# Performance work log

Hardware: AMD Instinct MI355X
Metric: run time of the kernel (lower is better)

Reference implementation:

```python
import jax, jax.numpy as jnp
import numpy as np

N_NODES = 100000


def _gcn_conv(x, W, b, src, dst, norm):
    # x: [N, Fin] -> [N, Fout]; PyG GCNConv: linear, normalized scatter-add, bias
    x = x @ W
    msgs = x[src] * norm[:, None]  # gather + edge scale
    out = jax.ops.segment_sum(msgs, dst, num_segments=N_NODES)
    return out + b


def setup_inputs() -> dict:
    key = jax.random.key(0)
    ks = jax.random.split(key, 8)
    N, E, F, H, C = N_NODES, 600000, 128, 128, 40
    s = lambda fan: 1.0 / np.sqrt(fan)
    return {
        "features": jax.random.normal(ks[0], (N, F), dtype=jnp.float32),
        "edge_index": jax.random.randint(ks[1], (2, E), 0, N, dtype=jnp.int64),
        "W1": jax.random.normal(ks[2], (F, H), dtype=jnp.float32) * s(F),
        "b1": jnp.zeros((H,), dtype=jnp.float32),
        "W2": jax.random.normal(ks[3], (H, H), dtype=jnp.float32) * s(H),
        "b2": jnp.zeros((H,), dtype=jnp.float32),
        "W3": jax.random.normal(ks[4], (H, C), dtype=jnp.float32) * s(H),
        "b3": jnp.zeros((C,), dtype=jnp.float32),
    }


def reference(features, edge_index, W1, b1, W2, b2, W3, b3):
    N = N_NODES
    # add self-loops (PyG GCNConv default)
    loops = jnp.arange(N, dtype=edge_index.dtype)
    src = jnp.concatenate([edge_index[0], loops])
    dst = jnp.concatenate([edge_index[1], loops])
    # symmetric normalization: deg^-1/2[src] * deg^-1/2[dst]
    deg = jax.ops.segment_sum(jnp.ones_like(dst, dtype=features.dtype), dst,
                              num_segments=N)
    dis = jnp.where(deg > 0, jax.lax.rsqrt(jnp.maximum(deg, 1.0)), 0.0)
    norm = dis[src] * dis[dst]

    x = jax.nn.relu(_gcn_conv(features, W1, b1, src, dst, norm))
    x = jax.nn.relu(_gcn_conv(x, W2, b2, src, dst, norm))
    x = jax.nn.relu(_gcn_conv(x, W3, b3, src, dst, norm))
    return jax.nn.log_softmax(x, axis=-1)
```

## Files before the change

### kernel.cpp

```cpp
#include <hip/hip_runtime.h>
#include <hip/hip_bf16.h>

#define NN 100000
#define NE 600000
#define NBLK 391
#define NPAD 100096

typedef unsigned int uint;
typedef unsigned short ushort;
typedef __attribute__((ext_vector_type(8))) short bf16x8;
typedef __attribute__((ext_vector_type(4))) float f32x4;

__device__ __forceinline__ ushort f2b(float f) {
    union { float f; uint u; } v; v.f = f;
    return (ushort)((v.u + 0x7fffu + ((v.u >> 16) & 1u)) >> 16);
}
__device__ __forceinline__ float b2f(uint h) {
    union { uint u; float f; } v; v.u = h << 16; return v.f;
}

__global__ __launch_bounds__(256) void k_cnt_init(int* __restrict__ cnt) {
    int i = blockIdx.x * 256 + threadIdx.x;
    if (i < NN) cnt[i] = 0;
}
__global__ __launch_bounds__(256) void k_cnt(const int* __restrict__ dst,
                                             int* __restrict__ cnt) {
    int e = blockIdx.x * 256 + threadIdx.x;
    if (e < NE) atomicAdd(&cnt[dst[e]], 1);
}
__global__ __launch_bounds__(256) void k_blockred(const int* __restrict__ cnt,
                                                  int* __restrict__ blocksum) {
    int t = threadIdx.x;
    int i = blockIdx.x * 256 + t;
    int c = (i < NN) ? cnt[i] : 0;
    #pragma unroll
    for (int o = 32; o; o >>= 1) c += __shfl_xor(c, o, 64);
    __shared__ int ws[4];
    if ((t & 63) == 0) ws[t >> 6] = c;
    __syncthreads();
    if (t == 0) blocksum[blockIdx.x] = ws[0] + ws[1] + ws[2] + ws[3];
}
__global__ __launch_bounds__(256) void k_scanblk(const int* __restrict__ blocksum,
                                                 int* __restrict__ blockbase) {
    __shared__ int s[NBLK];
    int t = threadIdx.x;
    for (int i = t; i < NBLK; i += 256) s[i] = blocksum[i];
    __syncthreads();
    if (t == 0) {
        int run = 0;
        for (int i = 0; i < NBLK; ++i) { int v = s[i]; s[i] = run; run += v; }
    }
    __syncthreads();
    for (int i = t; i < NBLK; i += 256) blockbase[i] = s[i];
}
__global__ __launch_bounds__(256) void k_offsets(const int* __restrict__ cnt,
                                                 const int* __restrict__ blockbase,
                                                 int* __restrict__ offsets,
                                                 int* __restrict__ cursor,
                                                 float* __restrict__ dis) {
    int t = threadIdx.x, lane = t & 63, wv = t >> 6;
    int i = blockIdx.x * 256 + t;
    int c = (i < NN) ? cnt[i] : 0;
    int x = c;
    #pragma unroll
    for (int o = 1; o < 64; o <<= 1) {
        int v = __shfl_up(x, o, 64);
        if (lane >= o) x += v;
    }
    __shared__ int wsum[4], wbase[4];
    if (lane == 63) wsum[wv] = x;
    __syncthreads();
    if (t == 0) {
        int run = 0;
        #pragma unroll
        for (int k = 0; k < 4; ++k) { wbase[k] = run; run += wsum[k]; }
    }
    __syncthreads();
    int excl = blockbase[blockIdx.x] + wbase[wv] + x - c;
    if (i < NN) {
        offsets[i] = excl;
        cursor[i] = excl;
        dis[i] = rsqrtf((float)(c + 1));
        if (i == NN - 1) offsets[NN] = excl + c;
    }
}
__global__ __launch_bounds__(256) void k_fill(const int* __restrict__ src,
                                              const int* __restrict__ dst,
                                              const float* __restrict__ dis,
                                              int* __restrict__ cursor,
                                              int2* __restrict__ edges) {
    int e = blockIdx.x * 256 + threadIdx.x;
    if (e < NE) {
        int s = src[e], d = dst[e];
        int pos = atomicAdd(&cursor[d], 1);
        float nr = dis[s] * dis[d];
        edges[pos] = make_int2(s, __float_as_int(nr));
    }
}

__global__ __launch_bounds__(256) void k_castW(const float* __restrict__ W1,
                                               const float* __restrict__ W2,
                                               const float* __restrict__ W3,
                                               ushort* __restrict__ WTall) {
    int o = blockIdx.x * 256 + threadIdx.x;
    if (o >= 38912) return;
    float v;
    if (o < 32768) {
        const float* W = (o < 16384) ? W1 : W2;
        int off = o & 16383;
        int n = off >> 7, k = off & 127;
        v = W[k * 128 + n];
    } else {
        int off = o - 32768;
        int n = off >> 7, k = off & 127;
        v = (n < 40) ? W3[k * 40 + n] : 0.f;
    }
    WTall[o] = f2b(v);
}

template <bool F32IN>
__global__ __launch_bounds__(256) void k_gemm128b(const void* __restrict__ Xin,
                                                  const ushort* __restrict__ WT,
                                                  ushort* __restrict__ Yb) {
    __shared__ ushort AL[64 * 136];
    __shared__ ushort BL[128 * 136];
    const int t = threadIdx.x;
    const int rbase = blockIdx.x * 64;
    #pragma unroll
    for (int i = 0; i < 8; ++i) {
        int ch = t + 256 * i;
        int n = ch >> 4, c = ch & 15;
        *(int4*)(BL + n * 136 + c * 8) = *(const int4*)(WT + n * 128 + c * 8);
    }
    #pragma unroll
    for (int i = 0; i < 4; ++i) {
        int ch = t + 256 * i;
        int m = ch >> 4, c = ch & 15;
        int row = min(rbase + m, NN - 1);
        if (F32IN) {
            const float* Xf = (const float*)Xin;
            float4 f0 = *(const float4*)(Xf + (size_t)row * 128 + c * 8);
            float4 f1 = *(const float4*)(Xf + (size_t)row * 128 + c * 8 + 4);
            ushort* p = AL + m * 136 + c * 8;
            p[0] = f2b(f0.x); p[1] = f2b(f0.y); p[2] = f2b(f0.z); p[3] = f2b(f0.w);
            p[4] = f2b(f1.x); p[5] = f2b(f1.y); p[6] = f2b(f1.z); p[7] = f2b(f1.w);
        } else {
            const ushort* Xb = (const ushort*)Xin;
            *(int4*)(AL + m * 136 + c * 8) =
                *(const int4*)(Xb + (size_t)row * 128 + c * 8);
        }
    }
    __syncthreads();
    const int wv = t >> 6, l = t & 63;
    const int m16 = l & 15, q = l >> 4;
    f32x4 acc[8];
    #pragma unroll
    for (int j = 0; j < 8; ++j) acc[j] = (f32x4){0.f, 0.f, 0.f, 0.f};
    #pragma unroll
    for (int kt = 0; kt < 4; ++kt) {
        bf16x8 a = *(const bf16x8*)(AL + (wv * 16 + m16) * 136 + kt * 32 + q * 8);
        #pragma unroll
        for (int j = 0; j < 8; ++j) {
            bf16x8 b = *(const bf16x8*)(BL + (j * 16 + m16) * 136 + kt * 32 + q * 8);
            acc[j] = __builtin_amdgcn_mfma_f32_16x16x32_bf16(a, b, acc[j], 0, 0, 0);
        }
    }
    #pragma unroll
    for (int r = 0; r < 4; ++r) {
        int row = rbase + wv * 16 + q * 4 + r;
        if (row < NN) {
            #pragma unroll
            for (int j = 0; j < 8; ++j)
                Yb[(size_t)row * 128 + j * 16 + m16] = f2b(acc[j][r]);
        }
    }
}

__global__ __launch_bounds__(256) void k_gemm40b(const ushort* __restrict__ Xb,
                                                 const ushort* __restrict__ W3T,
                                                 ushort* __restrict__ Yb) {
    __shared__ ushort AL[128 * 136];
    __shared__ ushort BL[48 * 136];
    const int t = threadIdx.x;
    const int rbase = blockIdx.x * 128;
    #pragma unroll
    for (int i = 0; i < 3; ++i) {
        int ch = t + 256 * i;
        int n = ch >> 4, c = ch & 15;
        *(int4*)(BL + n * 136 + c * 8) = *(const int4*)(W3T + n * 128 + c * 8);
    }
    #pragma unroll
    for (int i = 0; i < 8; ++i) {
        int ch = t + 256 * i;
        int m = ch >> 4, c = ch & 15;
        *(int4*)(AL + m * 136 + c * 8) =
            *(const int4*)(Xb + (size_t)(rbase + m) * 128 + c * 8);
    }
    __syncthreads();
    const int wv = t >> 6, l = t & 63;
    const int m16 = l & 15, q = l >> 4;
    f32x4 acc[2][3];
    #pragma unroll
    for (int i = 0; i < 2; ++i)
        #pragma unroll
        for (int j = 0; j < 3; ++j) acc[i][j] = (f32x4){0.f, 0.f, 0.f, 0.f};
    #pragma unroll
    for (int kt = 0; kt < 4; ++kt) {
        bf16x8 a[2], b[3];
        #pragma unroll
        for (int i = 0; i < 2; ++i)
            a[i] = *(const bf16x8*)(AL + ((wv * 2 + i) * 16 + m16) * 136 + kt * 32 + q * 8);
        #pragma unroll
        for (int j = 0; j < 3; ++j)
            b[j] = *(const bf16x8*)(BL + (j * 16 + m16) * 136 + kt * 32 + q * 8);
        #pragma unroll
        for (int i = 0; i < 2; ++i)
            #pragma unroll
            for (int j = 0; j < 3; ++j)
                acc[i][j] = __builtin_amdgcn_mfma_f32_16x16x32_bf16(a[i], b[j], acc[i][j], 0, 0, 0);
    }
    #pragma unroll
    for (int i = 0; i < 2; ++i) {
        #pragma unroll
        for (int r = 0; r < 4; ++r) {
            int row = rbase + (wv * 2 + i) * 16 + q * 4 + r;
            if (row < NN) {
                #pragma unroll
                for (int j = 0; j < 3; ++j)
                    Yb[(size_t)row * 64 + j * 16 + m16] = f2b(acc[i][j][r]);
            }
        }
    }
}

__global__ __launch_bounds__(256) void k_agg128b(const int* __restrict__ offsets,
                                                 const int2* __restrict__ edges,
                                                 const float* __restrict__ dis,
                                                 const ushort* __restrict__ xw,
                                                 const float* __restrict__ bias,
                                                 ushort* __restrict__ out) {
    const int t = threadIdx.x;
    const int wv = t >> 6, lane = t & 63;
    const int hl = lane & 31;
    const int hsel = lane & 32;
    const int n = (blockIdx.x * 4 + wv) * 2 + (lane >> 5);
    const bool nvalid = n < NN;
    const int nc = nvalid ? n : NN - 1;
    const int beg = offsets[nc], end = offsets[nc + 1];
    const int deg = end - beg;
    int2 em = (hl < deg) ? edges[beg + hl] : make_int2(0, 0);
    int s_l = em.x;
    float w_l = __int_as_float(em.y);
    float d = dis[nc];
    uint2 v0 = ((const uint2*)(xw + (size_t)nc * 128))[hl];
    float a0 = b2f(v0.x & 0xffffu) * (d * d);
    float a1 = b2f(v0.x >> 16) * (d * d);
    float a2 = b2f(v0.y & 0xffffu) * (d * d);
    float a3 = b2f(v0.y >> 16) * (d * d);
    int degc = min(deg, 32);
    int dmax = max(degc, __shfl_xor(degc, 32, 64));
    int jceil = (dmax + 7) & ~7;
    for (int j = 0; j < jceil; j += 8) {
        int s[8]; float w[8]; uint2 u[8];
        #pragma unroll
        for (int k = 0; k < 8; ++k) {
            s[k] = __shfl(s_l, hsel + j + k, 64);
            w[k] = __shfl(w_l, hsel + j + k, 64);
        }
        #pragma unroll
        for (int k = 0; k < 8; ++k)
            u[k] = ((const uint2*)(xw + (size_t)s[k] * 128))[hl];
        #pragma unroll
        for (int k = 0; k < 8; ++k) {
            a0 = fmaf(b2f(u[k].x & 0xffffu), w[k], a0);
            a1 = fmaf(b2f(u[k].x >> 16), w[k], a1);
            a2 = fmaf(b2f(u[k].y & 0xffffu), w[k], a2);
            a3 = fmaf(b2f(u[k].y >> 16), w[k], a3);
        }
    }
    for (int jj = beg + 32; jj < end; ++jj) {
        int2 e2 = edges[jj];
        float w = __int_as_float(e2.y);
        uint2 u = ((const uint2*)(xw + (size_t)e2.x * 128))[hl];
        a0 = fmaf(b2f(u.x & 0xffffu), w, a0);
        a1 = fmaf(b2f(u.x >> 16), w, a1);
        a2 = fmaf(b2f(u.y & 0xffffu), w, a2);
        a3 = fmaf(b2f(u.y >> 16), w, a3);
    }
    float4 bv = ((const float4*)bias)[hl];
    a0 = fmaxf(a0 + bv.x, 0.f);
    a1 = fmaxf(a1 + bv.y, 0.f);
    a2 = fmaxf(a2 + bv.z, 0.f);
    a3 = fmaxf(a3 + bv.w, 0.f);
    if (nvalid) {
        uint2 o;
        o.x = (uint)f2b(a0) | ((uint)f2b(a1) << 16);
        o.y = (uint)f2b(a2) | ((uint)f2b(a3) << 16);
        ((uint2*)(out + (size_t)n * 128))[hl] = o;
    }
}

__global__ __launch_bounds__(256) void k_agg40_lsm(const int* __restrict__ offsets,
                                                   const int2* __restrict__ edges,
                                                   const float* __restrict__ dis,
                                                   const ushort* __restrict__ xw,
                                                   const float* __restrict__ bias,
                                                   float* __restrict__ out) {
    const int t = threadIdx.x;
    const int wv = t >> 6, lane = t & 63;
    const int hl = lane & 31;
    const int hsel = lane & 32;
    const int n = (blockIdx.x * 4 + wv) * 2 + (lane >> 5);
    const bool nvalid = n < NN;
    const int nc = nvalid ? n : NN - 1;
    const bool act = hl < 20;
    const int beg = offsets[nc], end = offsets[nc + 1];
    const int deg = end - beg;
    int2 em = (hl < deg) ? edges[beg + hl] : make_int2(0, 0);
    int s_l = em.x;
    float w_l = __int_as_float(em.y);
    float d = dis[nc];
    uint v0 = ((const uint*)(xw + (size_t)nc * 64))[hl];
    float x0 = b2f(v0 & 0xffffu) * (d * d);
    float x1 = b2f(v0 >> 16) * (d * d);
    int degc = min(deg, 32);
    int dmax = max(degc, __shfl_xor(degc, 32, 64));
    int jceil = (dmax + 7) & ~7;
    for (int j = 0; j < jceil; j += 8) {
        int s[8]; float w[8]; uint u[8];
        #pragma unroll
        for (int k = 0; k < 8; ++k) {
            s[k] = __shfl(s_l, hsel + j + k, 64);
            w[k] = __shfl(w_l, hsel + j + k, 64);
        }
        #pragma unroll
        for (int k = 0; k < 8; ++k)
            u[k] = ((const uint*)(xw + (size_t)s[k] * 64))[hl];
        #pragma unroll
        for (int k = 0; k < 8; ++k) {
            x0 = fmaf(b2f(u[k] & 0xffffu), w[k], x0);
            x1 = fmaf(b2f(u[k] >> 16), w[k], x1);
        }
    }
    for (int jj = beg + 32; jj < end; ++jj) {
        int2 e2 = edges[jj];
        float w = __int_as_float(e2.y);
        uint u = ((const uint*)(xw + (size_t)e2.x * 64))[hl];
        x0 = fmaf(b2f(u & 0xffffu), w, x0);
        x1 = fmaf(b2f(u >> 16), w, x1);
    }
    if (act) {
        float2 bv = ((const float2*)bias)[hl];
        x0 = fmaxf(x0 + bv.x, 0.f);
        x1 = fmaxf(x1 + bv.y, 0.f);
    }
    float m = act ? fmaxf(x0, x1) : -1e30f;
    #pragma unroll
    for (int o = 16; o; o >>= 1) m = fmaxf(m, __shfl_xor(m, o, 64));
    float e = act ? (expf(x0 - m) + expf(x1 - m)) : 0.f;
    #pragma unroll
    for (int o = 16; o; o >>= 1) e += __shfl_xor(e, o, 64);
    if (act && nvalid) {
        float lg = m + logf(e);
        float2 o2 = make_float2(x0 - lg, x1 - lg);
        *(float2*)(out + (size_t)n * 40 + 2 * hl) = o2;
    }
}

extern "C" void kernel_launch(void* const* d_in, const int* in_sizes, int n_in,
                              void* d_out, int out_size, void* d_ws, size_t ws_size,
                              hipStream_t stream) {
    const float* feat = (const float*)d_in[0];
    const int* ei = (const int*)d_in[1];
    const float* W1 = (const float*)d_in[2];
    const float* b1 = (const float*)d_in[3];
    const float* W2 = (const float*)d_in[4];
    const float* b2 = (const float*)d_in[5];
    const float* W3 = (const float*)d_in[6];
    const float* b3 = (const float*)d_in[7];
    const int* src = ei;
    const int* dst = ei + NE;
    float* out = (float*)d_out;

    char* w = (char*)d_ws;
    int* cnt = (int*)w;        w += 100352 * 4;
    float* dis = (float*)w;    w += 100352 * 4;
    int* offsets = (int*)w;    w += 100608 * 4;
    int* cursor = (int*)w;     w += 100352 * 4;
    int* blocksum = (int*)w;   w += 512 * 4;
    int* blockbase = (int*)w;  w += 512 * 4;
    int2* edges = (int2*)w;    w += 600064 * 8;
    ushort* WTall = (ushort*)w; w += 39168 * 2;
    ushort* W1T = WTall;
    ushort* W2T = WTall + 16384;
    ushort* W3T = WTall + 32768;
    ushort* bufYb = (ushort*)w; w += (size_t)NPAD * 128 * 2;
    ushort* bufXb = (ushort*)w; w += (size_t)NPAD * 128 * 2;
    ushort* Y40b = (ushort*)w;  w += (size_t)NPAD * 64 * 2;

    const int B = 256;
    #define CDIV(a, b) (((a) + (b) - 1) / (b))

    k_cnt_init<<<NBLK, B, 0, stream>>>(cnt);
    k_cnt<<<CDIV(NE, B), B, 0, stream>>>(dst, cnt);
    k_blockred<<<NBLK, B, 0, stream>>>(cnt, blocksum);
    k_scanblk<<<1, B, 0, stream>>>(blocksum, blockbase);
    k_offsets<<<NBLK, B, 0, stream>>>(cnt, blockbase, offsets, cursor, dis);
    k_fill<<<CDIV(NE, B), B, 0, stream>>>(src, dst, dis, cursor, edges);
    k_castW<<<CDIV(38912, B), B, 0, stream>>>(W1, W2, W3, WTall);

    k_gemm128b<true><<<CDIV(NN, 64), B, 0, stream>>>(feat, W1T, bufYb);
    k_agg128b<<<CDIV(NN, 8), B, 0, stream>>>(offsets, edges, dis, bufYb, b1, bufXb);
    k_gemm128b<false><<<CDIV(NN, 64), B, 0, stream>>>(bufXb, W2T, bufYb);
    k_agg128b<<<CDIV(NN, 8), B, 0, stream>>>(offsets, edges, dis, bufYb, b2, bufXb);
    k_gemm40b<<<CDIV(NN, 128), B, 0, stream>>>(bufXb, W3T, Y40b);
    k_agg40_lsm<<<CDIV(NN, 8), B, 0, stream>>>(offsets, edges, dis, Y40b, b3, out);
    #undef CDIV
}
```

Baseline: 279.1 us.

## Use 16 lanes per node in 128-wide aggregation, fuse castW into scan kernel

The 128-feature aggregation kernel now assigns 16 lanes per node instead of 32, with each lane loading 16-byte (uint4) bf16 chunks and accumulating 8 features, so one wave handles four nodes. The edge window preloaded into lanes shrinks from 32 to 16, and higher-degree tails fall back to a serial loop. The weight cast kernel is merged into the single-block scan kernel as extra blocks to save a launch, and the fp32-to-bf16 staging in the first GEMM writes one 16-byte shared store instead of eight scalar stores. The wider per-lane gathers should cut instruction count per byte, at the cost of more work per lane and more nodes spilling into the serial tail loop.

```diff
diff --git a/kernel.cpp b/kernel.cpp
--- a/kernel.cpp
+++ b/kernel.cpp
@@ -14,6 +14,9 @@
 __device__ __forceinline__ ushort f2b(float f) {
     union { float f; uint u; } v; v.f = f;
     return (ushort)((v.u + 0x7fffu + ((v.u >> 16) & 1u)) >> 16);
+}
+__device__ __forceinline__ uint f2b2(float lo, float hi) {
+    return (uint)f2b(lo) | ((uint)f2b(hi) << 16);
 }
 __device__ __forceinline__ float b2f(uint h) {
     union { uint u; float f; } v; v.u = h << 16; return v.f;
@@ -40,18 +43,39 @@
     __syncthreads();
     if (t == 0) blocksum[blockIdx.x] = ws[0] + ws[1] + ws[2] + ws[3];
 }
-__global__ __launch_bounds__(256) void k_scanblk(const int* __restrict__ blocksum,
-                                                 int* __restrict__ blockbase) {
-    __shared__ int s[NBLK];
+__global__ __launch_bounds__(256) void k_scanblk_castW(const int* __restrict__ blocksum,
+                                                       int* __restrict__ blockbase,
+                                                       const float* __restrict__ W1,
+                                                       const float* __restrict__ W2,
+                                                       const float* __restrict__ W3,
+                                                       ushort* __restrict__ WTall) {
     int t = threadIdx.x;
-    for (int i = t; i < NBLK; i += 256) s[i] = blocksum[i];
-    __syncthreads();
-    if (t == 0) {
-        int run = 0;
-        for (int i = 0; i < NBLK; ++i) { int v = s[i]; s[i] = run; run += v; }
-    }
-    __syncthreads();
-    for (int i = t; i < NBLK; i += 256) blockbase[i] = s[i];
+    if (blockIdx.x == 0) {
+        __shared__ int s[NBLK];
+        for (int i = t; i < NBLK; i += 256) s[i] = blocksum[i];
+        __syncthreads();
+        if (t == 0) {
+            int run = 0;
+            for (int i = 0; i < NBLK; ++i) { int v = s[i]; s[i] = run; run += v; }
+        }
+        __syncthreads();
+        for (int i = t; i < NBLK; i += 256) blockbase[i] = s[i];
+    } else {
+        int o = (blockIdx.x - 1) * 256 + t;
+        if (o >= 38912) return;
+        float v;
+        if (o < 32768) {
+            const float* W = (o < 16384) ? W1 : W2;
+            int off = o & 16383;
+            int n = off >> 7, k = off & 127;
+            v = W[k * 128 + n];
+        } else {
+            int off = o - 32768;
+            int n = off >> 7, k = off & 127;
+            v = (n < 40) ? W3[k * 40 + n] : 0.f;
+        }
+        WTall[o] = f2b(v);
+    }
 }
 __global__ __launch_bounds__(256) void k_offsets(const int* __restrict__ cnt,
                                                  const int* __restrict__ blockbase,
@@ -98,26 +122,6 @@
     }
 }
 
-__global__ __launch_bounds__(256) void k_castW(const float* __restrict__ W1,
-                                               const float* __restrict__ W2,
-                                               const float* __restrict__ W3,
-                                               ushort* __restrict__ WTall) {
-    int o = blockIdx.x * 256 + threadIdx.x;
-    if (o >= 38912) return;
-    float v;
-    if (o < 32768) {
-        const float* W = (o < 16384) ? W1 : W2;
-        int off = o & 16383;
-        int n = off >> 7, k = off & 127;
-        v = W[k * 128 + n];
-    } else {
-        int off = o - 32768;
-        int n = off >> 7, k = off & 127;
-        v = (n < 40) ? W3[k * 40 + n] : 0.f;
-    }
-    WTall[o] = f2b(v);
-}
-
 template <bool F32IN>
 __global__ __launch_bounds__(256) void k_gemm128b(const void* __restrict__ Xin,
                                                   const ushort* __restrict__ WT,
@@ -141,9 +145,12 @@
             const float* Xf = (const float*)Xin;
             float4 f0 = *(const float4*)(Xf + (size_t)row * 128 + c * 8);
             float4 f1 = *(const float4*)(Xf + (size_t)row * 128 + c * 8 + 4);
-            ushort* p = AL + m * 136 + c * 8;
-            p[0] = f2b(f0.x); p[1] = f2b(f0.y); p[2] = f2b(f0.z); p[3] = f2b(f0.w);
-            p[4] = f2b(f1.x); p[5] = f2b(f1.y); p[6] = f2b(f1.z); p[7] = f2b(f1.w);
+            uint4 o;
+            o.x = f2b2(f0.x, f0.y);
+            o.y = f2b2(f0.z, f0.w);
+            o.z = f2b2(f1.x, f1.y);
+            o.w = f2b2(f1.z, f1.w);
+            *(uint4*)(AL + m * 136 + c * 8) = o;
         } else {
             const ushort* Xb = (const ushort*)Xin;
             *(int4*)(AL + m * 136 + c * 8) =
@@ -241,9 +248,9 @@
                                                  ushort* __restrict__ out) {
     const int t = threadIdx.x;
     const int wv = t >> 6, lane = t & 63;
-    const int hl = lane & 31;
-    const int hsel = lane & 32;
-    const int n = (blockIdx.x * 4 + wv) * 2 + (lane >> 5);
+    const int hl = lane & 15;
+    const int qsel = lane & 48;
+    const int n = (blockIdx.x * 4 + wv) * 4 + (lane >> 4);
     const bool nvalid = n < NN;
     const int nc = nvalid ? n : NN - 1;
     const int beg = offsets[nc], end = offsets[nc + 1];
@@ -252,51 +259,64 @@
     int s_l = em.x;
     float w_l = __int_as_float(em.y);
     float d = dis[nc];
-    uint2 v0 = ((const uint2*)(xw + (size_t)nc * 128))[hl];
-    float a0 = b2f(v0.x & 0xffffu) * (d * d);
-    float a1 = b2f(v0.x >> 16) * (d * d);
-    float a2 = b2f(v0.y & 0xffffu) * (d * d);
-    float a3 = b2f(v0.y >> 16) * (d * d);
-    int degc = min(deg, 32);
-    int dmax = max(degc, __shfl_xor(degc, 32, 64));
+    float dd = d * d;
+    uint4 v0 = ((const uint4*)(xw + (size_t)nc * 128))[hl];
+    float a0 = b2f(v0.x & 0xffffu) * dd, a1 = b2f(v0.x >> 16) * dd;
+    float a2 = b2f(v0.y & 0xffffu) * dd, a3 = b2f(v0.y >> 16) * dd;
+    float a4 = b2f(v0.z & 0xffffu) * dd, a5 = b2f(v0.z >> 16) * dd;
+    float a6 = b2f(v0.w & 0xffffu) * dd, a7 = b2f(v0.w >> 16) * dd;
+    int degc = min(deg, 16);
+    int m1 = max(degc, __shfl_xor(degc, 16, 64));
+    int dmax = max(m1, __shfl_xor(m1, 32, 64));
     int jceil = (dmax + 7) & ~7;
     for (int j = 0; j < jceil; j += 8) {
-        int s[8]; float w[8]; uint2 u[8];
+        int s[8]; float w[8]; uint4 u[8];
         #pragma unroll
         for (int k = 0; k < 8; ++k) {
-            s[k] = __shfl(s_l, hsel + j + k, 64);
-            w[k] = __shfl(w_l, hsel + j + k, 64);
+            s[k] = __shfl(s_l, qsel + j + k, 64);
+            w[k] = __shfl(w_l, qsel + j + k, 64);
         }
         #pragma unroll
         for (int k = 0; k < 8; ++k)
-            u[k] = ((const uint2*)(xw + (size_t)s[k] * 128))[hl];
+            u[k] = ((const uint4*)(xw + (size_t)s[k] * 128))[hl];
         #pragma unroll
         for (int k = 0; k < 8; ++k) {
             a0 = fmaf(b2f(u[k].x & 0xffffu), w[k], a0);
             a1 = fmaf(b2f(u[k].x >> 16), w[k], a1);
             a2 = fmaf(b2f(u[k].y & 0xffffu), w[k], a2);
             a3 = fmaf(b2f(u[k].y >> 16), w[k], a3);
-        }
-    }
-    for (int jj = beg + 32; jj < end; ++jj) {
+            a4 = fmaf(b2f(u[k].z & 0xffffu), w[k], a4);
+            a5 = fmaf(b2f(u[k].z >> 16), w[k], a5);
+            a6 = fmaf(b2f(u[k].w & 0xffffu), w[k], a6);
+            a7 = fmaf(b2f(u[k].w >> 16), w[k], a7);
+        }
+    }
+    for (int jj = beg + 16; jj < end; ++jj) {
         int2 e2 = edges[jj];
         float w = __int_as_float(e2.y);
-        uint2 u = ((const uint2*)(xw + (size_t)e2.x * 128))[hl];
+        uint4 u = ((const uint4*)(xw + (size_t)e2.x * 128))[hl];
         a0 = fmaf(b2f(u.x & 0xffffu), w, a0);
         a1 = fmaf(b2f(u.x >> 16), w, a1);
         a2 = fmaf(b2f(u.y & 0xffffu), w, a2);
         a3 = fmaf(b2f(u.y >> 16), w, a3);
-    }
-    float4 bv = ((const float4*)bias)[hl];
-    a0 = fmaxf(a0 + bv.x, 0.f);
-    a1 = fmaxf(a1 + bv.y, 0.f);
-    a2 = fmaxf(a2 + bv.z, 0.f);
-    a3 = fmaxf(a3 + bv.w, 0.f);
+        a4 = fmaf(b2f(u.z & 0xffffu), w, a4);
+        a5 = fmaf(b2f(u.z >> 16), w, a5);
+        a6 = fmaf(b2f(u.w & 0xffffu), w, a6);
+        a7 = fmaf(b2f(u.w >> 16), w, a7);
+    }
+    float4 bv0 = ((const float4*)bias)[2 * hl];
+    float4 bv1 = ((const float4*)bias)[2 * hl + 1];
+    a0 = fmaxf(a0 + bv0.x, 0.f); a1 = fmaxf(a1 + bv0.y, 0.f);
+    a2 = fmaxf(a2 + bv0.z, 0.f); a3 = fmaxf(a3 + bv0.w, 0.f);
+    a4 = fmaxf(a4 + bv1.x, 0.f); a5 = fmaxf(a5 + bv1.y, 0.f);
+    a6 = fmaxf(a6 + bv1.z, 0.f); a7 = fmaxf(a7 + bv1.w, 0.f);
     if (nvalid) {
-        uint2 o;
-        o.x = (uint)f2b(a0) | ((uint)f2b(a1) << 16);
-        o.y = (uint)f2b(a2) | ((uint)f2b(a3) << 16);
-        ((uint2*)(out + (size_t)n * 128))[hl] = o;
+        uint4 o;
+        o.x = f2b2(a0, a1);
+        o.y = f2b2(a2, a3);
+        o.z = f2b2(a4, a5);
+        o.w = f2b2(a6, a7);
+        ((uint4*)(out + (size_t)n * 128))[hl] = o;
     }
 }
 
@@ -404,15 +424,15 @@
     k_cnt_init<<<NBLK, B, 0, stream>>>(cnt);
     k_cnt<<<CDIV(NE, B), B, 0, stream>>>(dst, cnt);
     k_blockred<<<NBLK, B, 0, stream>>>(cnt, blocksum);
-    k_scanblk<<<1, B, 0, stream>>>(blocksum, blockbase);
+    k_scanblk_castW<<<1 + CDIV(38912, B), B, 0, stream>>>(blocksum, blockbase,
+                                                          W1, W2, W3, WTall);
     k_offsets<<<NBLK, B, 0, stream>>>(cnt, blockbase, offsets, cursor, dis);
     k_fill<<<CDIV(NE, B), B, 0, stream>>>(src, dst, dis, cursor, edges);
-    k_castW<<<CDIV(38912, B), B, 0, stream>>>(W1, W2, W3, WTall);
 
     k_gemm128b<true><<<CDIV(NN, 64), B, 0, stream>>>(feat, W1T, bufYb);
-    k_agg128b<<<CDIV(NN, 8), B, 0, stream>>>(offsets, edges, dis, bufYb, b1, bufXb);
+    k_agg128b<<<CDIV(NN, 16), B, 0, stream>>>(offsets, edges, dis, bufYb, b1, bufXb);
     k_gemm128b<false><<<CDIV(NN, 64), B, 0, stream>>>(bufXb, W2T, bufYb);
-    k_agg128b<<<CDIV(NN, 8), B, 0, stream>>>(offsets, edges, dis, bufYb, b2, bufXb);
+    k_agg128b<<<CDIV(NN, 16), B, 0, stream>>>(offsets, edges, dis, bufYb, b2, bufXb);
     k_gemm40b<<<CDIV(NN, 128), B, 0, stream>>>(bufXb, W3T, Y40b);
     k_agg40_lsm<<<CDIV(NN, 8), B, 0, stream>>>(offsets, edges, dis, Y40b, b3, out);
     #undef CDIV
```

After: 278.6 us. About the same (-0.1%).
